# Kernel tuning notes

Hardware: AMD Instinct MI355X
Metric: run time of the kernel (lower is better)

The kernel has to match this reference:

```python
import jax, jax.numpy as jnp
import numpy as np

B, S, D = 4, 2048, 1024   # batch, seq_len, input feature dim
H, E = 16, 64             # head_num, att_embedding_size; H*E = model dim


def setup_inputs() -> dict:
    key = jax.random.key(0)
    ks = jax.random.split(key, 9)
    std = 1.0 / np.sqrt(D)
    M = H * E
    return {
        "x": jax.random.normal(ks[0], (B, S, D), dtype=jnp.float32),
        "Wq": jax.random.normal(ks[1], (D, M), dtype=jnp.float32) * std,
        "bq": jnp.zeros((M,), dtype=jnp.float32),
        "Wk": jax.random.normal(ks[2], (D, M), dtype=jnp.float32) * std,
        "bk": jnp.zeros((M,), dtype=jnp.float32),
        "Wv": jax.random.normal(ks[3], (D, M), dtype=jnp.float32) * std,
        "bv": jnp.zeros((M,), dtype=jnp.float32),
        "Wr": jax.random.normal(ks[4], (D, M), dtype=jnp.float32) * std,
        "br": jnp.zeros((M,), dtype=jnp.float32),
    }


def reference(x, Wq, bq, Wk, bk, Wv, bv, Wr, br):
    # QKV dense layers with ReLU activation (as in the original Keras code)
    qw = jax.nn.relu(x @ Wq + bq)                      # [B,S,H*E]
    kw = jax.nn.relu(x @ Wk + bk)
    vw = jax.nn.relu(x @ Wv + bv)
    # split heads: [B,S,H,E] -> [B,H,S,E]
    qw = qw.reshape(B, S, H, E).transpose(0, 2, 1, 3)
    kw = kw.reshape(B, S, H, E).transpose(0, 2, 1, 3)
    vw = vw.reshape(B, S, H, E).transpose(0, 2, 1, 3)
    # unscaled attention (original has no 1/sqrt(d) scaling)
    a = jnp.einsum("bhqe,bhke->bhqk", qw, kw)          # [B,H,S,S]
    a = jax.nn.softmax(a, axis=-1)
    o = jnp.einsum("bhqk,bhke->bhqe", a, vw)           # [B,H,S,E]
    o = o.transpose(0, 2, 1, 3).reshape(B, S, H * E)
    # residual dense (no activation)
    o = o + (x @ Wr + br)
    return o
```

## Files before the change

### kernel.cpp

```cpp
#include <hip/hip_runtime.h>


typedef __bf16 bf16x8 __attribute__((ext_vector_type(8)));
typedef float  f32x4  __attribute__((ext_vector_type(4)));
typedef short  short8 __attribute__((ext_vector_type(8)));
typedef short  short4v __attribute__((ext_vector_type(4)));
typedef float  float4v __attribute__((ext_vector_type(4)));
typedef int    int4v  __attribute__((ext_vector_type(4)));
typedef unsigned uint2v __attribute__((ext_vector_type(2)));

#define LOG2E 1.44269504088896f

__device__ __forceinline__ unsigned short f2bf(float f) {
  unsigned u = __builtin_bit_cast(unsigned, f);
  u += 0x7fffu + ((u >> 16) & 1u);
  return (unsigned short)(u >> 16);
}

__device__ __forceinline__ unsigned pack2(float lo, float hi) {
  __bf16 a = (__bf16)lo, b = (__bf16)hi;
  unsigned short ua = __builtin_bit_cast(unsigned short, a);
  unsigned short ub = __builtin_bit_cast(unsigned short, b);
  return (unsigned)ua | ((unsigned)ub << 16);
}

__global__ __launch_bounds__(256) void k_cvt_x(const float* __restrict__ x,
                                               short* __restrict__ Xb) {
  const size_t i = ((size_t)blockIdx.x * 256 + threadIdx.x) * 4;
  float4v f = *(const float4v*)(x + i);
  short4v o;
  o[0] = (short)f2bf(f[0]); o[1] = (short)f2bf(f[1]);
  o[2] = (short)f2bf(f[2]); o[3] = (short)f2bf(f[3]);
  *(short4v*)(Xb + i) = o;
}

__global__ __launch_bounds__(256) void k_cvt_w(const float* __restrict__ Wq,
                                               const float* __restrict__ Wk,
                                               const float* __restrict__ Wv,
                                               const float* __restrict__ Wr,
                                               short* __restrict__ Wc) {
  const int bid = blockIdx.x;
  const int w = bid >> 8;
  const int t = bid & 255;
  const int tr = t >> 4, tc = t & 15;
  const float* Ws = (w == 0) ? Wq : (w == 1) ? Wk : (w == 2) ? Wv : Wr;
  __shared__ float T[64][65];
  const int tx = threadIdx.x & 63, ty = threadIdx.x >> 6;
#pragma unroll
  for (int i = 0; i < 16; ++i)
    T[i * 4 + ty][tx] = Ws[(size_t)(tr * 64 + i * 4 + ty) * 1024 + tc * 64 + tx];
  __syncthreads();
#pragma unroll
  for (int i = 0; i < 16; ++i) {
    const int n = tc * 64 + i * 4 + ty;
    Wc[((size_t)w * 1024 + n) * 1024 + tr * 64 + tx] = (short)f2bf(T[tx][i * 4 + ty]);
  }
}

__global__ __launch_bounds__(512, 2) void k_gemm(const short* __restrict__ Xb,
                                                 const short* __restrict__ Wc,
                                                 const float* __restrict__ bq,
                                                 const float* __restrict__ bk2,
                                                 const float* __restrict__ bv,
                                                 const float* __restrict__ br,
                                                 short* __restrict__ Qb,
                                                 short* __restrict__ Kb,
                                                 short* __restrict__ Vt,
                                                 float* __restrict__ Out) {
  __shared__ __align__(16) short smem[65536];
  char* const sb = (char*)smem;
  const int tid = threadIdx.x, wid = tid >> 6, lane = tid & 63;
  const int lr = lane & 15, hi = lane >> 4;
  const int bm = blockIdx.x & 31, bn = blockIdx.x >> 5;
  const int m0 = bm * 256, n0 = bn * 256;
  const int wm = wid >> 2, wn = wid & 3;

  f32x4 acc[8][4] = {};

  const int sl_ = (tid & 7) ^ ((tid >> 3) & 7);
  const int rA0 = ((tid >> 3) << 1) + (sl_ >> 2);
  const short* sa0 = Xb + (size_t)(m0 + rA0) * 1024 + (sl_ & 3) * 8;
  const short* sa1 = Xb + (size_t)(m0 + 128 + rA0) * 1024 + (sl_ & 3) * 8;
  const short* sg0 = Wc + (size_t)(n0 + rA0) * 1024 + (sl_ & 3) * 8;
  const short* sg1 = Wc + (size_t)(n0 + 128 + rA0) * 1024 + (sl_ & 3) * 8;

  const int xr = (((lane & 1) * 4 + hi) ^ ((lr >> 1) & 7)) * 16;
  const int amb = wm * 8192 + (lr >> 1) * 128 + xr;
  const int bnb = 65536 + wn * 4096 + (lr >> 1) * 128 + xr;

#define GLL(SRC, LDSOFF)                                                                   \
  __builtin_amdgcn_global_load_lds((const __attribute__((address_space(1))) void*)(SRC),   \
      (__attribute__((address_space(3))) void*)(sb + (LDSOFF)), 16, 0, 0)

#define STAGE(SLOT)                                                                        \
  do {                                                                                     \
    GLL(sa0, (SLOT) * 16384 + wid * 1024);                                                 \
    GLL(sa1, (SLOT) * 16384 + 8192 + wid * 1024);                                          \
    GLL(sg0, 65536 + (SLOT) * 16384 + wid * 1024);                                         \
    GLL(sg1, 65536 + (SLOT) * 16384 + 8192 + wid * 1024);                                  \
    sa0 += 32; sa1 += 32; sg0 += 32; sg1 += 32;                                            \
  } while (0)

#define PHASE(J, VM, STG)                                                                  \
  do {                                                                                     \
    asm volatile("s_waitcnt vmcnt(" #VM ")" ::: "memory");                                 \
    __builtin_amdgcn_sched_barrier(0);                                                     \
    __builtin_amdgcn_s_barrier();                                                          \
    __builtin_amdgcn_sched_barrier(0);                                                     \
    if (STG) STAGE(((J) + 3) & 3);                                                         \
    bf16x8 am[8], bnr[4];                                                                  \
    _Pragma("unroll")                                                                      \
    for (int mf = 0; mf < 8; ++mf)                                                         \
      am[mf] = *(const bf16x8*)(sb + (((J) & 3) * 16384 + amb + mf * 1024));               \
    _Pragma("unroll")                                                                      \
    for (int nf = 0; nf < 4; ++nf)                                                         \
      bnr[nf] = *(const bf16x8*)(sb + (((J) & 3) * 16384 + bnb + nf * 1024));              \
    asm volatile("s_waitcnt lgkmcnt(0)" ::: "memory");                                     \
    __builtin_amdgcn_sched_barrier(0);                                                     \
    __builtin_amdgcn_s_setprio(1);                                                         \
    _Pragma("unroll")                                                                      \
    for (int mf = 0; mf < 8; ++mf)                                                         \
      _Pragma("unroll")                                                                    \
      for (int nf = 0; nf < 4; ++nf)                                                       \
        acc[mf][nf] = __builtin_amdgcn_mfma_f32_16x16x32_bf16(am[mf], bnr[nf],             \
                                                              acc[mf][nf], 0, 0, 0);      \
    __builtin_amdgcn_s_setprio(0);                                                         \
    __builtin_amdgcn_sched_barrier(0);                                                     \
  } while (0)

  STAGE(0);
  STAGE(1);
  STAGE(2);

  for (int it = 0; it < 7; ++it) {
    PHASE(0, 8, 1);
    PHASE(1, 8, 1);
    PHASE(2, 8, 1);
    PHASE(3, 8, 1);
  }
  PHASE(0, 8, 1);
  PHASE(1, 8, 0);
  PHASE(2, 4, 0);
  PHASE(3, 0, 0);
#undef PHASE
#undef STAGE
#undef GLL

#pragma unroll
  for (int mf = 0; mf < 8; ++mf) {
    const int mbase = m0 + wm * 128 + mf * 16 + hi * 4;
    const int bb2 = mbase >> 11, sbase = mbase & 2047;
#pragma unroll
    for (int nf = 0; nf < 4; ++nf) {
      const int n = n0 + wn * 64 + nf * 16 + lr;
      const float* bp = (n < 2048) ? (n < 1024 ? bq : bk2) : (n < 3072 ? bv : br);
      const float bias = bp[n & 1023];
      float v[4];
#pragma unroll
      for (int r = 0; r < 4; ++r) v[r] = acc[mf][nf][r] + bias;

      if (n < 2048) {
        const int nn = n & 1023, h = nn >> 6, e = nn & 63;
        short* dst = (n < 1024) ? Qb : Kb;
        const float scale = (n < 1024) ? LOG2E : 1.0f;
#pragma unroll
        for (int r = 0; r < 4; ++r)
          dst[(((size_t)bb2 * 16 + h) * 2048 + sbase + r) * 64 + e] =
              (short)f2bf(fmaxf(v[r], 0.f) * scale);
      } else if (n < 3072) {
        const int nn = n & 1023, h = nn >> 6, e = nn & 63;
        const int kq = sbase & 31;
        const int Sp = (sbase & ~31) + ((kq >> 2) & 3) * 8 + (kq >> 4) * 4;
        uint2v pv;
        pv[0] = pack2(fmaxf(v[0], 0.f), fmaxf(v[1], 0.f));
        pv[1] = pack2(fmaxf(v[2], 0.f), fmaxf(v[3], 0.f));
        *(uint2v*)&Vt[(((size_t)bb2 * 16 + h) * 64 + e) * 2048 + Sp] = pv;
      } else {
#pragma unroll
        for (int r = 0; r < 4; ++r)
          Out[(size_t)(mbase + r) * 1024 + (n - 3072)] = v[r];
      }
    }
  }
}

__global__ __launch_bounds__(256, 4) void k_attn(const short* __restrict__ Qb,
                                                 const short* __restrict__ Kb,
                                                 const short* __restrict__ Vt,
                                                 float* __restrict__ Out) {
  __shared__ __align__(16) short smem[16384];
  char* const sb = (char*)smem;
  const int tid = threadIdx.x, wid = tid >> 6, lane = tid & 63;
  const int lr = lane & 15, hi = lane >> 4;
  const int bid = ((blockIdx.x & 7) << 7) | (blockIdx.x >> 3);
  const int bh = bid >> 4;
  const int q0 = (bid & 15) * 128;
  const size_t hb = (size_t)bh * (2048 * 64);

  bf16x8 aq[2][2];
#pragma unroll
  for (int g = 0; g < 2; ++g) {
    const short* qp = Qb + hb + (size_t)(q0 + wid * 32 + g * 16 + lr) * 64 + hi * 8;
    aq[g][0] = *(const bf16x8*)qp;
    aq[g][1] = *(const bf16x8*)(qp + 32);
  }

  f32x4 o[2][4] = {};
  float l_run[2] = {0.f, 0.f};

  const int swz = ((lane & 7) ^ (lane >> 3)) * 8;
  const int rlo = lane >> 3;
  const int wr0 = wid * 16;
  const short* kp0 = Kb + hb + (size_t)(wr0 + rlo) * 64 + swz;
  const short* kp1 = kp0 + 8 * 64;
  const short* vp0 = Vt + hb + (size_t)(wr0 + rlo) * 2048 + swz;
  const short* vp1 = vp0 + 8 * 2048;

  const int vb0 = (lr * 64 + ((hi ^ (lr & 7)) << 3)) * 2;
  const int vb1 = vb0 ^ 64;

#define GLL(SRC, LDSOFF)                                                                   \
  __builtin_amdgcn_global_load_lds((const __attribute__((address_space(1))) void*)(SRC),   \
      (__attribute__((address_space(3))) void*)(sb + (LDSOFF)), 16, 0, 0)

  GLL(kp0, wr0 * 128);
  GLL(kp1, wr0 * 128 + 1024);
  GLL(vp0, 16384 + wr0 * 128);
  GLL(vp1, 16384 + wr0 * 128 + 1024);
  kp0 += 4096; kp1 += 4096; vp0 += 64; vp1 += 64;

  for (int kt = 0; kt < 32; ++kt) {
    const int buf = kt & 1;
    if (kt < 31) {
      const int d = (buf ^ 1) * 8192 + wr0 * 128;
      GLL(kp0, d);
      GLL(kp1, d + 1024);
      GLL(vp0, 16384 + d);
      GLL(vp1, 16384 + d + 1024);
      kp0 += 4096; kp1 += 4096; vp0 += 64; vp1 += 64;
      asm volatile("s_waitcnt vmcnt(4)" ::: "memory");
    } else {
      asm volatile("s_waitcnt vmcnt(0)" ::: "memory");
    }
    __builtin_amdgcn_sched_barrier(0);
    __builtin_amdgcn_s_barrier();
    __builtin_amdgcn_sched_barrier(0);

    f32x4 s[2][4];
    __builtin_amdgcn_s_setprio(1);
#pragma unroll
    for (int kc = 0; kc < 4; ++kc) {
      const bf16x8 kf0 = *(const bf16x8*)(sb + (vb0 + buf * 8192 + kc * 2048));
      const bf16x8 kf1 = *(const bf16x8*)(sb + (vb1 + buf * 8192 + kc * 2048));
      f32x4 t0 = __builtin_amdgcn_mfma_f32_16x16x32_bf16(kf0, aq[0][0], (f32x4){0.f, 0.f, 0.f, 0.f}, 0, 0, 0);
      s[0][kc] = __builtin_amdgcn_mfma_f32_16x16x32_bf16(kf1, aq[0][1], t0, 0, 0, 0);
      f32x4 t1 = __builtin_amdgcn_mfma_f32_16x16x32_bf16(kf0, aq[1][0], (f32x4){0.f, 0.f, 0.f, 0.f}, 0, 0, 0);
      s[1][kc] = __builtin_amdgcn_mfma_f32_16x16x32_bf16(kf1, aq[1][1], t1, 0, 0, 0);
    }
    __builtin_amdgcn_s_setprio(0);

    int4v pw[2][2];
#pragma unroll
    for (int g = 0; g < 2; ++g) {
      float sum = 0.f;
#pragma unroll
      for (int kc = 0; kc < 4; ++kc) {
        const float p0 = __builtin_amdgcn_exp2f(s[g][kc][0]);
        const float p1 = __builtin_amdgcn_exp2f(s[g][kc][1]);
        const float p2 = __builtin_amdgcn_exp2f(s[g][kc][2]);
        const float p3 = __builtin_amdgcn_exp2f(s[g][kc][3]);
        sum += (p0 + p1) + (p2 + p3);
        pw[g][kc >> 1][(kc & 1) * 2] = (int)pack2(p0, p1);
        pw[g][kc >> 1][(kc & 1) * 2 + 1] = (int)pack2(p2, p3);
      }
      l_run[g] += sum;
    }

    __builtin_amdgcn_s_setprio(1);
#pragma unroll
    for (int kk = 0; kk < 2; ++kk) {
      const bf16x8 pa0 = __builtin_bit_cast(bf16x8, pw[0][kk]);
      const bf16x8 pa1 = __builtin_bit_cast(bf16x8, pw[1][kk]);
      const int cb = (kk ? vb1 : vb0) + 16384 + buf * 8192;
#pragma unroll
      for (int et = 0; et < 4; ++et) {
        const bf16x8 vf = *(const bf16x8*)(sb + (cb + et * 2048));
        o[0][et] = __builtin_amdgcn_mfma_f32_16x16x32_bf16(vf, pa0, o[0][et], 0, 0, 0);
        o[1][et] = __builtin_amdgcn_mfma_f32_16x16x32_bf16(vf, pa1, o[1][et], 0, 0, 0);
      }
    }
    __builtin_amdgcn_s_setprio(0);

    asm volatile("s_waitcnt lgkmcnt(0)" ::: "memory");
    __builtin_amdgcn_sched_barrier(0);
    __builtin_amdgcn_s_barrier();
    __builtin_amdgcn_sched_barrier(0);
  }

  float* Ep = (float*)smem + wid * 1088;
  const int b = bh >> 4, h = bh & 15;
  const int qr = lane >> 2, cc = lane & 3;
#pragma unroll
  for (int g = 0; g < 2; ++g) {
    float lt = l_run[g];
    lt += __shfl_xor(lt, 16);
    lt += __shfl_xor(lt, 32);
    const float inv = 1.0f / lt;
#pragma unroll
    for (int et = 0; et < 4; ++et) {
      f32x4 v = o[g][et] * inv;
      *(float4v*)&Ep[lr * 68 + et * 16 + hi * 4] = v;
    }
    asm volatile("s_waitcnt lgkmcnt(0)" ::: "memory");
    const size_t gb = ((size_t)b * 2048 + q0 + wid * 32 + g * 16 + qr) * 1024 + h * 64 + cc * 4;
#pragma unroll
    for (int i = 0; i < 4; ++i) {
      float4v v = *(const float4v*)&Ep[qr * 68 + cc * 4 + i * 16];
      float4v u = *(const float4v*)&Out[gb + i * 16];
      u += v;
      *(float4v*)&Out[gb + i * 16] = u;
    }
    asm volatile("s_waitcnt lgkmcnt(0)" ::: "memory");
  }
#undef GLL
}

extern "C" void kernel_launch(void* const* d_in, const int* in_sizes, int n_in,
                              void* d_out, int out_size, void* d_ws, size_t ws_size,
                              hipStream_t stream) {
  const float* x  = (const float*)d_in[0];
  const float* Wq = (const float*)d_in[1];
  const float* bq = (const float*)d_in[2];
  const float* Wk = (const float*)d_in[3];
  const float* bk = (const float*)d_in[4];
  const float* Wv = (const float*)d_in[5];
  const float* bv = (const float*)d_in[6];
  const float* Wr = (const float*)d_in[7];
  const float* br = (const float*)d_in[8];
  float* Out = (float*)d_out;

  char* ws = (char*)d_ws;
  short* Xb = (short*)(ws);
  short* Wc = (short*)(ws + (size_t)16 * 1024 * 1024);
  short* Qb = (short*)(ws + (size_t)24 * 1024 * 1024);
  short* Kb = (short*)(ws + (size_t)40 * 1024 * 1024);
  short* Vt = (short*)(ws + (size_t)56 * 1024 * 1024);

  k_cvt_x<<<8192, 256, 0, stream>>>(x, Xb);
  k_cvt_w<<<1024, 256, 0, stream>>>(Wq, Wk, Wv, Wr, Wc);
  k_gemm<<<512, 512, 0, stream>>>(Xb, Wc, bq, bk, bv, br, Qb, Kb, Vt, Out);
  k_attn<<<1024, 256, 0, stream>>>(Qb, Kb, Vt, Out);
}
```

Measured before the change: 166.9 us.

## Restructure attention K/V pipeline into four-slot 32-key stages with one barrier

The attention loop moves from double-buffered 64-key tiles with two barriers per tile to a 4-slot ring of 32-key stages, prefetched three stages ahead with a single barrier per stage. The K/V LDS layouts and swizzles are rewritten so each wave loads one 16-byte chunk per tensor per stage. The aim is to hide global load latency more deeply and remove one barrier per step. In exchange there are twice as many barrier phases with smaller MFMA batches per phase, and the hand-computed vmcnt counts must match the number of loads in flight.

```diff
diff --git a/kernel.cpp b/kernel.cpp
--- a/kernel.cpp
+++ b/kernel.cpp
@@ -207,95 +207,114 @@
 
   f32x4 o[2][4] = {};
   float l_run[2] = {0.f, 0.f};
-
-  const int swz = ((lane & 7) ^ (lane >> 3)) * 8;
+  f32x4 s[2][2];
+  const f32x4 z4 = {0.f, 0.f, 0.f, 0.f};
+
   const int rlo = lane >> 3;
-  const int wr0 = wid * 16;
-  const short* kp0 = Kb + hb + (size_t)(wr0 + rlo) * 64 + swz;
-  const short* kp1 = kp0 + 8 * 64;
-  const short* vp0 = Vt + hb + (size_t)(wr0 + rlo) * 2048 + swz;
-  const short* vp1 = vp0 + 8 * 2048;
-
-  const int vb0 = (lr * 64 + ((hi ^ (lr & 7)) << 3)) * 2;
-  const int vb1 = vb0 ^ 64;
+  const int kswz = ((lane & 7) ^ rlo) * 8;
+  const short* kp = Kb + hb + (size_t)(wid * 8 + rlo) * 64 + kswz;
+  const int vl = (lane & 7) ^ rlo;
+  const int ve = 2 * (wid * 8 + rlo) + (vl >> 2);
+  const short* vp = Vt + hb + (size_t)ve * 2048 + (vl & 3) * 8;
+
+  const int kb0 = lr * 128 + ((hi ^ (lr & 7)) << 4);
+  const int kb1 = kb0 ^ 64;
+  const int vvb = (lr >> 1) * 128 + ((((lr & 1) * 4 + hi) ^ ((lr >> 1) & 7)) << 4);
 
 #define GLL(SRC, LDSOFF)                                                                   \
   __builtin_amdgcn_global_load_lds((const __attribute__((address_space(1))) void*)(SRC),   \
       (__attribute__((address_space(3))) void*)(sb + (LDSOFF)), 16, 0, 0)
 
-  GLL(kp0, wr0 * 128);
-  GLL(kp1, wr0 * 128 + 1024);
-  GLL(vp0, 16384 + wr0 * 128);
-  GLL(vp1, 16384 + wr0 * 128 + 1024);
-  kp0 += 4096; kp1 += 4096; vp0 += 64; vp1 += 64;
-
-  for (int kt = 0; kt < 32; ++kt) {
-    const int buf = kt & 1;
-    if (kt < 31) {
-      const int d = (buf ^ 1) * 8192 + wr0 * 128;
-      GLL(kp0, d);
-      GLL(kp1, d + 1024);
-      GLL(vp0, 16384 + d);
-      GLL(vp1, 16384 + d + 1024);
-      kp0 += 4096; kp1 += 4096; vp0 += 64; vp1 += 64;
-      asm volatile("s_waitcnt vmcnt(4)" ::: "memory");
-    } else {
-      asm volatile("s_waitcnt vmcnt(0)" ::: "memory");
-    }
-    __builtin_amdgcn_sched_barrier(0);
-    __builtin_amdgcn_s_barrier();
-    __builtin_amdgcn_sched_barrier(0);
-
-    f32x4 s[2][4];
-    __builtin_amdgcn_s_setprio(1);
-#pragma unroll
-    for (int kc = 0; kc < 4; ++kc) {
-      const bf16x8 kf0 = *(const bf16x8*)(sb + (vb0 + buf * 8192 + kc * 2048));
-      const bf16x8 kf1 = *(const bf16x8*)(sb + (vb1 + buf * 8192 + kc * 2048));
-      f32x4 t0 = __builtin_amdgcn_mfma_f32_16x16x32_bf16(kf0, aq[0][0], (f32x4){0.f, 0.f, 0.f, 0.f}, 0, 0, 0);
-      s[0][kc] = __builtin_amdgcn_mfma_f32_16x16x32_bf16(kf1, aq[0][1], t0, 0, 0, 0);
-      f32x4 t1 = __builtin_amdgcn_mfma_f32_16x16x32_bf16(kf0, aq[1][0], (f32x4){0.f, 0.f, 0.f, 0.f}, 0, 0, 0);
-      s[1][kc] = __builtin_amdgcn_mfma_f32_16x16x32_bf16(kf1, aq[1][1], t1, 0, 0, 0);
-    }
-    __builtin_amdgcn_s_setprio(0);
-
-    int4v pw[2][2];
-#pragma unroll
-    for (int g = 0; g < 2; ++g) {
-      float sum = 0.f;
-#pragma unroll
-      for (int kc = 0; kc < 4; ++kc) {
-        const float p0 = __builtin_amdgcn_exp2f(s[g][kc][0]);
-        const float p1 = __builtin_amdgcn_exp2f(s[g][kc][1]);
-        const float p2 = __builtin_amdgcn_exp2f(s[g][kc][2]);
-        const float p3 = __builtin_amdgcn_exp2f(s[g][kc][3]);
-        sum += (p0 + p1) + (p2 + p3);
-        pw[g][kc >> 1][(kc & 1) * 2] = (int)pack2(p0, p1);
-        pw[g][kc >> 1][(kc & 1) * 2 + 1] = (int)pack2(p2, p3);
-      }
-      l_run[g] += sum;
-    }
-
-    __builtin_amdgcn_s_setprio(1);
-#pragma unroll
-    for (int kk = 0; kk < 2; ++kk) {
-      const bf16x8 pa0 = __builtin_bit_cast(bf16x8, pw[0][kk]);
-      const bf16x8 pa1 = __builtin_bit_cast(bf16x8, pw[1][kk]);
-      const int cb = (kk ? vb1 : vb0) + 16384 + buf * 8192;
-#pragma unroll
-      for (int et = 0; et < 4; ++et) {
-        const bf16x8 vf = *(const bf16x8*)(sb + (cb + et * 2048));
-        o[0][et] = __builtin_amdgcn_mfma_f32_16x16x32_bf16(vf, pa0, o[0][et], 0, 0, 0);
-        o[1][et] = __builtin_amdgcn_mfma_f32_16x16x32_bf16(vf, pa1, o[1][et], 0, 0, 0);
-      }
-    }
-    __builtin_amdgcn_s_setprio(0);
-
-    asm volatile("s_waitcnt lgkmcnt(0)" ::: "memory");
-    __builtin_amdgcn_sched_barrier(0);
-    __builtin_amdgcn_s_barrier();
-    __builtin_amdgcn_sched_barrier(0);
-  }
+#define ASTAGE(SLOT)                                                                       \
+  do {                                                                                     \
+    GLL(kp, (SLOT) * 4096 + wid * 1024);                                                   \
+    GLL(vp, 16384 + (SLOT) * 4096 + wid * 1024);                                           \
+    kp += 2048; vp += 32;                                                                  \
+  } while (0)
+
+#define APH(J, VM, STG)                                                                    \
+  do {                                                                                     \
+    asm volatile("s_waitcnt vmcnt(" #VM ") lgkmcnt(0)" ::: "memory");                      \
+    __builtin_amdgcn_sched_barrier(0);                                                     \
+    __builtin_amdgcn_s_barrier();                                                          \
+    __builtin_amdgcn_sched_barrier(0);                                                     \
+    if (STG) ASTAGE(((J) + 3) & 3);                                                        \
+    __builtin_amdgcn_s_setprio(1);                                                         \
+    _Pragma("unroll")                                                                      \
+    for (int kc = 0; kc < 2; ++kc) {                                                       \
+      const bf16x8 kf0 = *(const bf16x8*)(sb + ((J) * 4096 + kc * 2048 + kb0));            \
+      const bf16x8 kf1 = *(const bf16x8*)(sb + ((J) * 4096 + kc * 2048 + kb1));            \
+      f32x4 t0 = __builtin_amdgcn_mfma_f32_16x16x32_bf16(kf0, aq[0][0], z4, 0, 0, 0);      \
+      s[0][kc] = __builtin_amdgcn_mfma_f32_16x16x32_bf16(kf1, aq[0][1], t0, 0, 0, 0);      \
+      f32x4 t1 = __builtin_amdgcn_mfma_f32_16x16x32_bf16(kf0, aq[1][0], z4, 0, 0, 0);      \
+      s[1][kc] = __builtin_amdgcn_mfma_f32_16x16x32_bf16(kf1, aq[1][1], t1, 0, 0, 0);      \
+    }                                                                                      \
+    __builtin_amdgcn_s_setprio(0);                                                         \
+    int4v pw0, pw1;                                                                        \
+    {                                                                                      \
+      float sum0 = 0.f, sum1 = 0.f;                                                        \
+      {                                                                                    \
+        const float a0 = __builtin_amdgcn_exp2f(s[0][0][0]);                               \
+        const float a1 = __builtin_amdgcn_exp2f(s[0][0][1]);                               \
+        const float a2 = __builtin_amdgcn_exp2f(s[0][0][2]);                               \
+        const float a3 = __builtin_amdgcn_exp2f(s[0][0][3]);                               \
+        const float a4 = __builtin_amdgcn_exp2f(s[0][1][0]);                               \
+        const float a5 = __builtin_amdgcn_exp2f(s[0][1][1]);                               \
+        const float a6 = __builtin_amdgcn_exp2f(s[0][1][2]);                               \
+        const float a7 = __builtin_amdgcn_exp2f(s[0][1][3]);                               \
+        sum0 = ((a0 + a1) + (a2 + a3)) + ((a4 + a5) + (a6 + a7));                          \
+        pw0[0] = (int)pack2(a0, a1); pw0[1] = (int)pack2(a2, a3);                          \
+        pw0[2] = (int)pack2(a4, a5); pw0[3] = (int)pack2(a6, a7);                          \
+      }                                                                                    \
+      {                                                                                    \
+        const float b0 = __builtin_amdgcn_exp2f(s[1][0][0]);                               \
+        const float b1 = __builtin_amdgcn_exp2f(s[1][0][1]);                               \
+        const float b2 = __builtin_amdgcn_exp2f(s[1][0][2]);                               \
+        const float b3 = __builtin_amdgcn_exp2f(s[1][0][3]);                               \
+        const float b4 = __builtin_amdgcn_exp2f(s[1][1][0]);                               \
+        const float b5 = __builtin_amdgcn_exp2f(s[1][1][1]);                               \
+        const float b6 = __builtin_amdgcn_exp2f(s[1][1][2]);                               \
+        const float b7 = __builtin_amdgcn_exp2f(s[1][1][3]);                               \
+        sum1 = ((b0 + b1) + (b2 + b3)) + ((b4 + b5) + (b6 + b7));                          \
+        pw1[0] = (int)pack2(b0, b1); pw1[1] = (int)pack2(b2, b3);                          \
+        pw1[2] = (int)pack2(b4, b5); pw1[3] = (int)pack2(b6, b7);                          \
+      }                                                                                    \
+      l_run[0] += sum0; l_run[1] += sum1;                                                  \
+    }                                                                                      \
+    const bf16x8 pa0 = __builtin_bit_cast(bf16x8, pw0);                                    \
+    const bf16x8 pa1 = __builtin_bit_cast(bf16x8, pw1);                                    \
+    __builtin_amdgcn_s_setprio(1);                                                         \
+    _Pragma("unroll")                                                                      \
+    for (int et = 0; et < 4; ++et) {                                                       \
+      const bf16x8 vf = *(const bf16x8*)(sb + (16384 + (J) * 4096 + et * 1024 + vvb));     \
+      o[0][et] = __builtin_amdgcn_mfma_f32_16x16x32_bf16(vf, pa0, o[0][et], 0, 0, 0);      \
+      o[1][et] = __builtin_amdgcn_mfma_f32_16x16x32_bf16(vf, pa1, o[1][et], 0, 0, 0);      \
+    }                                                                                      \
+    __builtin_amdgcn_s_setprio(0);                                                         \
+  } while (0)
+
+  ASTAGE(0);
+  ASTAGE(1);
+  ASTAGE(2);
+
+  for (int it = 0; it < 15; ++it) {
+    APH(0, 4, 1);
+    APH(1, 4, 1);
+    APH(2, 4, 1);
+    APH(3, 4, 1);
+  }
+  APH(0, 4, 1);
+  APH(1, 4, 0);
+  APH(2, 2, 0);
+  APH(3, 0, 0);
+#undef APH
+#undef ASTAGE
+#undef GLL
+
+  asm volatile("s_waitcnt vmcnt(0) lgkmcnt(0)" ::: "memory");
+  __builtin_amdgcn_sched_barrier(0);
+  __builtin_amdgcn_s_barrier();
+  __builtin_amdgcn_sched_barrier(0);
 
   float* Ep = (float*)smem + wid * 1088;
   const int b = bh >> 4, h = bh & 15;
@@ -322,7 +341,6 @@
     }
     asm volatile("s_waitcnt lgkmcnt(0)" ::: "memory");
   }
-#undef GLL
 }
 
 extern "C" void kernel_launch(void* const* d_in, const int* in_sizes, int n_in,
```

After: 472.9 us. 2.83x slower.
